# Performance work log

Measured on AMD Instinct MI355X. Metric: run time of the kernel, lower is better.

Reference implementation:

```python
import jax, jax.numpy as jnp
import numpy as np

# Norse default LIFParameters
TAU_SYN_INV = 200.0  # 1/5e-3
TAU_MEM_INV = 100.0  # 1/1e-2
V_LEAK = 0.0
V_TH = 1.0
V_RESET = 0.0
DT = 0.001


def _heaviside(x):
    return (x > 0).astype(x.dtype)


def setup_inputs() -> dict:
    key = jax.random.key(0)
    k1, k2 = jax.random.split(key)
    T, B, F = 1024, 256, 512
    input_spikes = (jax.random.uniform(k1, (T, B, F)) < 0.1).astype(jnp.float32)
    W = jax.random.normal(k2, (F, F), dtype=jnp.float32) / np.sqrt(F).astype(np.float32)
    return {"input_spikes": input_spikes, "W": W}


def reference(input_spikes, W):
    # input_spikes: [T, B, F]; W: [F, F] (Linear, no bias)
    T, B, F = input_spikes.shape
    # fc batched across the whole sequence (y = x @ W.T)
    xs = jnp.einsum('tbf,gf->tbg', input_spikes, W)  # [T, B, F]
    v0 = jnp.zeros((B, F), dtype=input_spikes.dtype)
    i0 = jnp.zeros((B, F), dtype=input_spikes.dtype)

    def step(carry, x):
        v, i = carry
        v_dec = v + DT * TAU_MEM_INV * ((V_LEAK - v) + i)  # membrane leak+integrate
        i_dec = i - DT * TAU_SYN_INV * i                   # synaptic current decay
        z = _heaviside(v_dec - V_TH)                       # spike
        v_new = (1.0 - z) * v_dec + z * V_RESET            # reset
        i_new = i_dec + x                                  # inject fc output
        return (v_new, i_new), z

    (v, i), zs = jax.lax.scan(step, (v0, i0), xs)
    # matches torch forward: returns (z_last, state) with state = (v, i)
    return zs[-1], v, i
```

## Files before the change

kernel.cpp:

```cpp
#include <hip/hip_runtime.h>
#include <hip/hip_bf16.h>


typedef __attribute__((ext_vector_type(8))) short short8;
typedef __attribute__((ext_vector_type(4))) float floatx4;
typedef __attribute__((ext_vector_type(2))) unsigned uintx2;
typedef __attribute__((ext_vector_type(4))) int int4v;

#define T_STEPS 1024
#define B_DIM   256
#define F_DIM   512
#define BF      (B_DIM * F_DIM)
#define ROWP    520

static __device__ __forceinline__ unsigned short f2bf_rne(float f) {
    unsigned u = __float_as_uint(f);
    return (unsigned short)((u + 0x7FFFu + ((u >> 16) & 1u)) >> 16);
}
static __device__ __forceinline__ float bf2f(unsigned short h) {
    return __uint_as_float(((unsigned)h) << 16);
}

__global__ __launch_bounds__(256)
void pack_kernel(const float* __restrict__ sp, unsigned* __restrict__ bits)
{
    const int lane = threadIdx.x & 63;
    const int wv   = blockIdx.x * 4 + (threadIdx.x >> 6);
    for (int c = wv; c < 65536; c += 2048 * 4) {
        const float* p = sp + (size_t)c * 2048;
        unsigned val = 0;
        #pragma unroll
        for (int r = 0; r < 32; ++r) {
            float x = p[r * 64 + lane];
            unsigned long long m = __ballot(x != 0.0f);
            unsigned sel = (lane & 1) ? (unsigned)(m >> 32) : (unsigned)m;
            if ((lane >> 1) == r) val = sel;
        }
        bits[(size_t)c * 64 + lane] = val;
    }
}

__global__ __launch_bounds__(512, 4)
void lif_kernel_bits(const unsigned* __restrict__ bits,
                     const float* __restrict__ W,
                     float* __restrict__ out)
{
    __shared__ int   xq[8][4][512];
    __shared__ float rowmax[8][16];

    const int tid  = threadIdx.x;
    const int lane = tid & 63;
    const int wq   = tid >> 6;
    const int bt   = blockIdx.x & 15;
    const int gb   = blockIdx.x >> 4;
    const int b0   = bt * 16;
    const int gw   = gb * 16;
    const int mrow = lane & 15;
    const int lq   = lane >> 4;

    int4v wi0, wi1, wi2;
    float invC;
    {
        const float* wp = W + (size_t)(gw + mrow) * F_DIM + wq * 64 + lq * 16;
        float wv[16];
        float lm = 0.0f;
        #pragma unroll
        for (int j = 0; j < 16; ++j) {
            wv[j] = wp[j];
            lm = fmaxf(lm, fabsf(wv[j]));
        }
        lm = fmaxf(lm, __shfl_xor(lm, 16, 64));
        lm = fmaxf(lm, __shfl_xor(lm, 32, 64));
        if (lane < 16) rowmax[wq][lane] = lm;
        __syncthreads();
        float S = 1e-30f;
        #pragma unroll
        for (int w8 = 0; w8 < 8; ++w8) S = fmaxf(S, rowmax[w8][mrow]);
        __syncthreads();
        const float C = 8000000.0f / S;
        invC = S / 8000000.0f;
        #pragma unroll
        for (int d = 0; d < 4; ++d) {
            unsigned p0 = 0, p1 = 0, p2 = 0;
            #pragma unroll
            for (int jj = 0; jj < 4; ++jj) {
                int q  = __float2int_rn(wv[d * 4 + jj] * C);
                int d2 = (q << 24) >> 24;
                int r1 = (q - d2) >> 8;
                int d1 = (r1 << 24) >> 24;
                int d0 = (r1 - d1) >> 8;
                p0 |= (unsigned)(d0 & 0xFF) << (8 * jj);
                p1 |= (unsigned)(d1 & 0xFF) << (8 * jj);
                p2 |= (unsigned)(d2 & 0xFF) << (8 * jj);
            }
            wi0[d] = (int)p0; wi1[d] = (int)p1; wi2[d] = (int)p2;
        }
    }

    const bool fin  = (wq < 4);
    const int  rown = wq & 3;
    float v0 = 0.f, c0 = 0.f, z0 = 0.f;

    const unsigned* bp = bits + (size_t)(b0 + mrow) * 16 + wq * 2 + (lq >> 1);
    const int hsh = (lq & 1) * 16;

    auto ldbits = [&](int t) -> unsigned {
        return bp[(size_t)t * 4096];
    };

    auto expand = [&](unsigned dw) -> int4v {
        unsigned h16 = dw >> hsh;
        int4v a;
        #pragma unroll
        for (int d = 0; d < 4; ++d) {
            unsigned b4 = (h16 >> (4 * d)) & 0xFu;
            a[d] = (int)((b4 * 0x00204081u) & 0x01010101u);
        }
        return a;
    };

    const int4v iz = {0, 0, 0, 0};

    auto mci = [&](int4v aI) -> int4v {
        int4v a0 = __builtin_amdgcn_mfma_i32_16x16x64_i8(aI, wi0, iz, 0, 0, 0);
        int4v a1 = __builtin_amdgcn_mfma_i32_16x16x64_i8(aI, wi1, iz, 0, 0, 0);
        int4v a2 = __builtin_amdgcn_mfma_i32_16x16x64_i8(aI, wi2, iz, 0, 0, 0);
        int4v c;
        #pragma unroll
        for (int r = 0; r < 4; ++r)
            c[r] = ((a0[r] << 16) + (a1[r] << 8)) + a2[r];
        return c;
    };

    auto wrpart = [&](int slot, int4v c) {
        #pragma unroll
        for (int r = 0; r < 4; ++r)
            xq[slot][r][wq * 64 + lane] = c[r];
    };

    auto lif1 = [&](int slot) {
        const int* p = &xq[slot][rown][lane];
        int s = 0;
        #pragma unroll
        for (int w8 = 0; w8 < 8; ++w8)
            s += p[w8 * 64];
        float x  = (float)s * invC;
        float vd = v0 + 0.1f * ((0.0f - v0) + c0);
        float id = c0 - 0.2f * c0;
        bool  sp = (vd - 1.0f) > 0.0f;
        z0 = sp ? 1.0f : 0.0f;
        v0 = sp ? 0.0f : vd;
        c0 = id + x;
    };

    unsigned q0 = ldbits(0), q1 = ldbits(1), q2 = ldbits(2), q3 = ldbits(3);

    for (int t = 0; t < T_STEPS; t += 4) {
        const int sw = t & 4;
        const int sr = 4 - sw;

        int4v aA = expand(q0);
        int4v aB = expand(q1);
        int4v aC = expand(q2);
        int4v aD = expand(q3);
        if (t + 4 < T_STEPS) {
            q0 = ldbits(t + 4);
            q1 = ldbits(t + 5);
            q2 = ldbits(t + 6);
            q3 = ldbits(t + 7);
        }
        wrpart(sw + 0, mci(aA));
        wrpart(sw + 1, mci(aB));
        wrpart(sw + 2, mci(aC));
        wrpart(sw + 3, mci(aD));

        if (fin && t > 0) {
            lif1(sr + 0);
            lif1(sr + 1);
            lif1(sr + 2);
            lif1(sr + 3);
        }
        __syncthreads();
    }
    if (fin) {
        lif1(4);
        lif1(5);
        lif1(6);
        lif1(7);
        const size_t idx = (size_t)(b0 + lq * 4 + rown) * F_DIM + gw + mrow;
        out[idx]          = z0;
        out[BF + idx]     = v0;
        out[2 * BF + idx] = c0;
    }
}

__global__ __launch_bounds__(256, 1)
void lif_kernel_f32(const float* __restrict__ spikes,
                    const float* __restrict__ W,
                    float* __restrict__ out)
{
    __shared__ unsigned short sAf[16 * ROWP];
    __shared__ float xbuf[2 * 256];

    const int tid  = threadIdx.x;
    const int lane = tid & 63;
    const int w    = tid >> 6;
    const int gh   = w & 1;
    const int kh   = w >> 1;
    const int bt   = blockIdx.x & 15;
    const int gb   = blockIdx.x >> 4;
    const int b0   = bt * 16;
    const int gw   = gb * 32 + gh * 16;
    const int mrow = lane & 15;
    const int kq   = lane >> 4;

    short8 whi[8], wmd[8], wlo[8];
    {
        const float* wp = W + (size_t)(gw + mrow) * F_DIM + kh * 256 + kq * 8;
        #pragma unroll
        for (int ks = 0; ks < 8; ++ks) {
            short8 hi, md, lo;
            #pragma unroll
            for (int j = 0; j < 8; ++j) {
                float f = wp[ks * 32 + j];
                unsigned short h = f2bf_rne(f);
                float r1 = f - bf2f(h);
                unsigned short m = f2bf_rne(r1);
                float r2 = r1 - bf2f(m);
                hi[j] = (short)h;
                md[j] = (short)m;
                lo[j] = (short)f2bf_rne(r2);
            }
            whi[ks] = hi; wmd[ks] = md; wlo[ks] = lo;
        }
    }

    float v[4]  = {0.f, 0.f, 0.f, 0.f};
    float cu[4] = {0.f, 0.f, 0.f, 0.f};
    float zf[4] = {0.f, 0.f, 0.f, 0.f};

    floatx4 ld[8];
    auto issue_loads = [&](int t) {
        const floatx4* sp = (const floatx4*)(spikes + (size_t)t * BF + (size_t)b0 * F_DIM);
        #pragma unroll
        for (int j = 0; j < 8; ++j)
            ld[j] = sp[tid + 256 * j];
    };

    issue_loads(0);
    for (int t = 0; t < T_STEPS; ++t) {
        #pragma unroll
        for (int j = 0; j < 8; ++j) {
            const int q = tid + 256 * j;
            const int row = q >> 7, col4 = q & 127;
            unsigned u0 = __float_as_uint(ld[j][0]);
            unsigned u1 = __float_as_uint(ld[j][1]);
            unsigned u2 = __float_as_uint(ld[j][2]);
            unsigned u3 = __float_as_uint(ld[j][3]);
            uintx2 d;
            d[0] = (u0 >> 16) | (u1 & 0xFFFF0000u);
            d[1] = (u2 >> 16) | (u3 & 0xFFFF0000u);
            *(uintx2*)&sAf[row * ROWP + col4 * 4] = d;
        }
        __syncthreads();
        if (t + 1 < T_STEPS) issue_loads(t + 1);

        floatx4 ah = {0.f, 0.f, 0.f, 0.f};
        floatx4 am = {0.f, 0.f, 0.f, 0.f};
        floatx4 al = {0.f, 0.f, 0.f, 0.f};
        const unsigned short* arow = &sAf[mrow * ROWP + kh * 256 + kq * 8];
        #pragma unroll
        for (int ks = 0; ks < 8; ++ks) {
            short8 a = *(const short8*)(arow + ks * 32);
            ah = __builtin_amdgcn_mfma_f32_16x16x32_bf16(a, whi[ks], ah, 0, 0, 0);
            am = __builtin_amdgcn_mfma_f32_16x16x32_bf16(a, wmd[ks], am, 0, 0, 0);
            al = __builtin_amdgcn_mfma_f32_16x16x32_bf16(a, wlo[ks], al, 0, 0, 0);
        }

        if (kh == 1) {
            floatx4 xp = (ah + am) + al;
            *(floatx4*)&xbuf[gh * 256 + lane * 4] = xp;
        }
        __syncthreads();
        if (kh == 0) {
            floatx4 other = *(const floatx4*)&xbuf[gh * 256 + lane * 4];
            #pragma unroll
            for (int r = 0; r < 4; ++r) {
                float x    = ((ah[r] + am[r]) + al[r]) + other[r];
                float vdec = v[r] + 0.1f * ((0.0f - v[r]) + cu[r]);
                float idec = cu[r] - 0.2f * cu[r];
                bool  spk  = (vdec - 1.0f) > 0.0f;
                zf[r] = spk ? 1.0f : 0.0f;
                v[r]  = spk ? 0.0f : vdec;
                cu[r] = idec + x;
            }
        }
    }

    if (kh == 0) {
        #pragma unroll
        for (int r = 0; r < 4; ++r) {
            const size_t idx = (size_t)(b0 + kq * 4 + r) * F_DIM + gw + mrow;
            out[idx]          = zf[r];
            out[BF + idx]     = v[r];
            out[2 * BF + idx] = cu[r];
        }
    }
}

extern "C" void kernel_launch(void* const* d_in, const int* in_sizes, int n_in,
                              void* d_out, int out_size, void* d_ws, size_t ws_size,
                              hipStream_t stream)
{
    const float* spikes = (const float*)d_in[0];
    const float* W      = (const float*)d_in[1];
    float* out          = (float*)d_out;

    const size_t need_bits = (size_t)T_STEPS * B_DIM * (F_DIM / 8);

    if (d_ws != nullptr && ws_size >= need_bits) {
        unsigned* bits = (unsigned*)d_ws;
        pack_kernel<<<dim3(2048), dim3(256), 0, stream>>>(spikes, bits);
        lif_kernel_bits<<<dim3(512), dim3(512), 0, stream>>>(bits, W, out);
    } else {
        lif_kernel_f32<<<dim3(256), dim3(256), 0, stream>>>(spikes, W, out);
    }
}
```

Measured before the change: 1.144 ms.

## Halve pipeline chunk to two steps and write partial sums as vector stores

The time loop now handles two timesteps per barrier instead of four, using a four-slot ring buffer in shared memory. The layout changes so each lane writes its four MFMA accumulator rows as one 16-byte store. LIF reduction reads are remapped to match. This cuts LDS store instructions and shrinks the shared buffer, which may help occupancy, but it doubles the number of __syncthreads calls and shortens the overlap between loading and computing.

```diff
diff --git a/kernel.cpp b/kernel.cpp
--- a/kernel.cpp
+++ b/kernel.cpp
@@ -45,7 +45,7 @@
                      const float* __restrict__ W,
                      float* __restrict__ out)
 {
-    __shared__ int   xq[8][4][512];
+    __shared__ int   xq[4][8 * 256];
     __shared__ float rowmax[8][16];
 
     const int tid  = threadIdx.x;
@@ -132,18 +132,12 @@
         return c;
     };
 
-    auto wrpart = [&](int slot, int4v c) {
-        #pragma unroll
-        for (int r = 0; r < 4; ++r)
-            xq[slot][r][wq * 64 + lane] = c[r];
-    };
-
-    auto lif1 = [&](int slot) {
-        const int* p = &xq[slot][rown][lane];
+    auto lif1 = [&](const int* xs) {
+        const int* p = xs + lane * 4 + rown;
         int s = 0;
         #pragma unroll
         for (int w8 = 0; w8 < 8; ++w8)
-            s += p[w8 * 64];
+            s += p[w8 * 256];
         float x  = (float)s * invC;
         float vd = v0 + 0.1f * ((0.0f - v0) + c0);
         float id = c0 - 0.2f * c0;
@@ -153,40 +147,29 @@
         c0 = id + x;
     };
 
-    unsigned q0 = ldbits(0), q1 = ldbits(1), q2 = ldbits(2), q3 = ldbits(3);
-
-    for (int t = 0; t < T_STEPS; t += 4) {
-        const int sw = t & 4;
-        const int sr = 4 - sw;
-
-        int4v aA = expand(q0);
-        int4v aB = expand(q1);
-        int4v aC = expand(q2);
-        int4v aD = expand(q3);
-        if (t + 4 < T_STEPS) {
-            q0 = ldbits(t + 4);
-            q1 = ldbits(t + 5);
-            q2 = ldbits(t + 6);
-            q3 = ldbits(t + 7);
-        }
-        wrpart(sw + 0, mci(aA));
-        wrpart(sw + 1, mci(aB));
-        wrpart(sw + 2, mci(aC));
-        wrpart(sw + 3, mci(aD));
-
+    unsigned q0 = ldbits(0);
+    unsigned q1 = ldbits(1);
+
+    for (int t = 0; t < T_STEPS; t += 2) {
         if (fin && t > 0) {
-            lif1(sr + 0);
-            lif1(sr + 1);
-            lif1(sr + 2);
-            lif1(sr + 3);
+            lif1(&xq[(t + 2) & 3][0]);
+            lif1(&xq[(t + 3) & 3][0]);
+        }
+        {
+            int4v cA = mci(expand(q0));
+            *(int4v*)&xq[t & 3][wq * 256 + lane * 4] = cA;
+            int4v cB = mci(expand(q1));
+            *(int4v*)&xq[(t + 1) & 3][wq * 256 + lane * 4] = cB;
+        }
+        if (t + 2 < T_STEPS) {
+            q0 = ldbits(t + 2);
+            q1 = ldbits(t + 3);
         }
         __syncthreads();
     }
     if (fin) {
-        lif1(4);
-        lif1(5);
-        lif1(6);
-        lif1(7);
+        lif1(&xq[2][0]);
+        lif1(&xq[3][0]);
         const size_t idx = (size_t)(b0 + lq * 4 + rown) * F_DIM + gw + mrow;
         out[idx]          = z0;
         out[BF + idx]     = v0;
```

Result: no change. 1.151 ms (+0.6%).
